# Kernel optimization log

Hardware: AMD Instinct MI355X
Metric: run time of the kernel (lower is better)

Reference implementation:

```python
import jax, jax.numpy as jnp
import numpy as np

N_USERS = 100000
N_MOVIES = 20000
N_EDGES = 600000
FEAT = 64
HID = 128
OUT = 64
N_TUPLES = 100000


def _sage(x_src, x_dst, src_idx, dst_idx, n_dst, Wl, bl, Wr):
    # PyG SAGEConv (mean aggr): lin_l(mean of gathered src feats) + lin_r(x_dst)
    msg = x_src[src_idx]                                        # [E, d_src]
    summ = jax.ops.segment_sum(msg, dst_idx, num_segments=n_dst)
    cnt = jax.ops.segment_sum(jnp.ones((src_idx.shape[0],), x_src.dtype),
                              dst_idx, num_segments=n_dst)
    mean = summ / jnp.maximum(cnt, 1.0)[:, None]
    return mean @ Wl.T + bl + x_dst @ Wr.T


def setup_inputs() -> dict:
    key = jax.random.key(0)
    ks = jax.random.split(key, 20)
    s = 0.05
    return {
        "movie_x": jax.random.normal(ks[0], (N_MOVIES, FEAT), jnp.float32),
        "user_idx": jax.random.randint(ks[1], (N_EDGES,), 0, N_USERS),
        "movie_idx": jax.random.randint(ks[2], (N_EDGES,), 0, N_MOVIES),
        "tuples_coo": jax.random.randint(ks[3], (2, N_TUPLES), 0, N_MOVIES),
        "user_emb": jax.random.normal(ks[4], (1, HID), jnp.float32) * s,
        "W1l": jax.random.normal(ks[5], (HID, FEAT), jnp.float32) * s,
        "b1": jnp.zeros((HID,), jnp.float32),
        "W1r": jax.random.normal(ks[6], (HID, HID), jnp.float32) * s,
        "W2l": jax.random.normal(ks[7], (HID, HID), jnp.float32) * s,
        "b2": jnp.zeros((HID,), jnp.float32),
        "W2r": jax.random.normal(ks[8], (HID, FEAT), jnp.float32) * s,
        "W3l": jax.random.normal(ks[9], (HID, HID), jnp.float32) * s,
        "b3": jnp.zeros((HID,), jnp.float32),
        "W3r": jax.random.normal(ks[10], (HID, HID), jnp.float32) * s,
        "Wlin1": jax.random.normal(ks[11], (OUT, HID), jnp.float32) * s,
        "blin1": jnp.zeros((OUT,), jnp.float32),
        "Wlin2": jax.random.normal(ks[12], (OUT, HID), jnp.float32) * s,
        "blin2": jnp.zeros((OUT,), jnp.float32),
    }


def reference(movie_x, user_idx, movie_idx, tuples_coo, user_emb,
              W1l, b1, W1r, W2l, b2, W2r, W3l, b3, W3r,
              Wlin1, blin1, Wlin2, blin2):
    n_users = N_USERS
    user_x0 = jnp.broadcast_to(user_emb, (n_users, HID))  # emb.weight.repeat
    # conv1: (movie -> user) rev_rates edges: src=movie_idx, dst=user_idx
    user_x = jax.nn.relu(_sage(movie_x, user_x0, movie_idx, user_idx, n_users, W1l, b1, W1r))
    # conv2: (user -> movie) rates edges: src=user_idx, dst=movie_idx
    movie_z = jax.nn.relu(_sage(user_x, movie_x, user_idx, movie_idx, N_MOVIES, W2l, b2, W2r))
    # conv3: (movie -> user) again
    user_z = jax.nn.relu(_sage(movie_z, user_x, movie_idx, user_idx, n_users, W3l, b3, W3r))
    z_user = user_z @ Wlin1.T + blin1
    z_movie = movie_z @ Wlin2.T + blin2
    X = jnp.vstack((z_user, z_movie))
    # relation_schema = ['user', 'movie']: offset movie indices by n_users
    new_index = jnp.vstack((tuples_coo[0], tuples_coo[1] + n_users))
    return X, new_index
```

## Files before the change

kernel.cpp:

```cpp
#include <hip/hip_runtime.h>

typedef __attribute__((ext_vector_type(8))) short short8;
typedef __attribute__((ext_vector_type(4))) float f32x4;

static const int NU = 100000;
static const int NM = 20000;
static const int NE = 600000;
static const int FEAT = 64;
static const int HID = 128;
static const int OUTD = 64;
static const int NTOT = NU + NM;
static const int NLIST = 2 * NE;
static const int CVT_TOT = 81920 + NM * FEAT;
static const int CVT_BLKS = (CVT_TOT + 255) / 256;
static const int IDX_BLKS = (100000 + 255) / 256;

static const int UB_SHIFT = 9;
static const int MB_SHIFT = 7;
static const int NBU = (NU + 511) >> 9;
static const int NBM = (NM + 127) >> 7;
static const int NBUCK = NBU + NBM;
static const int EPB = 4096;
static const int NPBLK = (NE + EPB - 1) / EPB;

__device__ inline float b2f(unsigned short h) {
    unsigned int u = ((unsigned int)h) << 16;
    float f; __builtin_memcpy(&f, &u, 4); return f;
}
__device__ inline unsigned short f2b(float f) {
    unsigned int u; __builtin_memcpy(&u, &f, 4);
    u += 0x7FFFu + ((u >> 16) & 1u);
    return (unsigned short)(u >> 16);
}
__device__ inline unsigned int pk2(float a, float b) {
    return (unsigned int)f2b(a) | ((unsigned int)f2b(b) << 16);
}
__device__ inline int wswz(int row, int bc, int rowbytes) {
    return row * rowbytes + (bc ^ ((row & 7) << 4));
}

__global__ __launch_bounds__(256) void k_hist(const int* __restrict__ ui,
                                              const int* __restrict__ mi,
                                              int* __restrict__ ghist) {
    __shared__ int h[NBUCK];
    const int tid = threadIdx.x;
    for (int i = tid; i < NBUCK; i += 256) h[i] = 0;
    __syncthreads();
#pragma unroll
    for (int it = 0; it < EPB / 256; ++it) {
        int e = blockIdx.x * EPB + it * 256 + tid;
        if (e < NE) {
            atomicAdd(&h[ui[e] >> UB_SHIFT], 1);
            atomicAdd(&h[NBU + (mi[e] >> MB_SHIFT)], 1);
        }
    }
    __syncthreads();
    for (int i = tid; i < NBUCK; i += 256)
        if (h[i]) atomicAdd(&ghist[i], h[i]);
}

__global__ __launch_bounds__(512) void k_bscan(const int* __restrict__ ghist,
                                               int* __restrict__ bb,
                                               int* __restrict__ gcur) {
    __shared__ int s[512];
    const int tid = threadIdx.x;
    int v = (tid < NBUCK) ? ghist[tid] : 0;
    s[tid] = v;
    __syncthreads();
#pragma unroll
    for (int off = 1; off < 512; off <<= 1) {
        int x = (tid >= off) ? s[tid - off] : 0;
        __syncthreads();
        s[tid] += x;
        __syncthreads();
    }
    int excl = s[tid] - v;
    if (tid < NBUCK) { bb[tid] = excl; gcur[tid] = excl; }
    if (tid == 511) bb[NBUCK] = s[511];
}

__global__ __launch_bounds__(256) void k_part(const int* __restrict__ ui,
                                              const int* __restrict__ mi,
                                              int* __restrict__ gcur,
                                              int* __restrict__ entries) {
    __shared__ int h[NBUCK], base[NBUCK], cur[NBUCK];
    const int tid = threadIdx.x;
    for (int i = tid; i < NBUCK; i += 256) h[i] = 0;
    __syncthreads();

    int eu[EPB / 256], em[EPB / 256];
#pragma unroll
    for (int it = 0; it < EPB / 256; ++it) {
        int e = blockIdx.x * EPB + it * 256 + tid;
        if (e < NE) {
            eu[it] = ui[e]; em[it] = mi[e];
            atomicAdd(&h[eu[it] >> UB_SHIFT], 1);
            atomicAdd(&h[NBU + (em[it] >> MB_SHIFT)], 1);
        } else eu[it] = -1;
    }
    __syncthreads();
    for (int i = tid; i < NBUCK; i += 256) {
        int c = h[i];
        base[i] = c ? atomicAdd(&gcur[i], c) : 0;
        cur[i] = 0;
    }
    __syncthreads();
#pragma unroll
    for (int it = 0; it < EPB / 256; ++it) {
        if (eu[it] < 0) continue;
        int u = eu[it], m = em[it];
        int bu = u >> UB_SHIFT;
        int o1 = base[bu] + atomicAdd(&cur[bu], 1);
        entries[o1] = (m << UB_SHIFT) | (u & 511);
        int bm = NBU + (m >> MB_SHIFT);
        int o2 = base[bm] + atomicAdd(&cur[bm], 1);
        entries[o2] = (u << MB_SHIFT) | (m & 127);
    }
}

__global__ __launch_bounds__(256) void k_csr(const int* __restrict__ bb,
                                             const int* __restrict__ entries,
                                             int* __restrict__ rp,
                                             int* __restrict__ list) {
    __shared__ int lcnt[512], lrp[512], lcur[512], ps[256];
    const int b = blockIdx.x;
    const int tid = threadIdx.x;
    const int s = bb[b], e = bb[b + 1];
    const bool isU = b < NBU;
    const int shift = isU ? UB_SHIFT : MB_SHIFT;
    const int mask = isU ? 511 : 127;
    const int n0 = isU ? (b << UB_SHIFT) : ((b - NBU) << MB_SHIFT);
    const int nNodes = isU ? min(512, NU - n0) : min(128, NM - n0);
    const int g0 = isU ? n0 : NU + n0;

    for (int i = tid; i < 512; i += 256) { lcnt[i] = 0; lcur[i] = 0; }
    __syncthreads();
    for (int i = s + tid; i < e; i += 256)
        atomicAdd(&lcnt[entries[i] & mask], 1);
    __syncthreads();
    int a0 = lcnt[2 * tid], a1 = lcnt[2 * tid + 1];
    int pr = a0 + a1;
    ps[tid] = pr;
    __syncthreads();
#pragma unroll
    for (int off = 1; off < 256; off <<= 1) {
        int x = (tid >= off) ? ps[tid - off] : 0;
        __syncthreads();
        ps[tid] += x;
        __syncthreads();
    }
    int excl = ps[tid] - pr;
    lrp[2 * tid] = excl;
    lrp[2 * tid + 1] = excl + a0;
    __syncthreads();
    for (int i = tid; i < nNodes; i += 256) rp[g0 + i] = s + lrp[i];
    if (b == NBUCK - 1 && tid == 0) rp[NTOT] = e;
    for (int i = s + tid; i < e; i += 256) {
        int p = entries[i];
        int dl = p & mask;
        int off = s + lrp[dl] + atomicAdd(&lcur[dl], 1);
        list[off] = p >> shift;
    }
}

__global__ void k_misc(const float* __restrict__ w1l, const float* __restrict__ w2l,
                       const float* __restrict__ w2r, const float* __restrict__ w3l,
                       const float* __restrict__ w3r, const float* __restrict__ wl1,
                       const float* __restrict__ wl2, const float* __restrict__ mx,
                       unsigned short* __restrict__ dst,
                       const int* __restrict__ tpl, float* __restrict__ oidx,
                       const float* __restrict__ ue, const float* __restrict__ w1r,
                       const float* __restrict__ b1, float* __restrict__ c1) {
    const int b = blockIdx.x;
    if (b < CVT_BLKS) {
        int g = b * 256 + threadIdx.x;
        if (g >= CVT_TOT) return;
        const float* s; int o;
        if      (g < 8192)   { s = w1l; o = g; }
        else if (g < 24576)  { s = w2l; o = g - 8192; }
        else if (g < 32768)  { s = w2r; o = g - 24576; }
        else if (g < 49152)  { s = w3l; o = g - 32768; }
        else if (g < 65536)  { s = w3r; o = g - 49152; }
        else if (g < 73728)  { s = wl1; o = g - 65536; }
        else if (g < 81920)  { s = wl2; o = g - 73728; }
        else                 { s = mx;  o = g - 81920; }
        dst[g] = f2b(s[o]);
    } else if (b < CVT_BLKS + IDX_BLKS) {
        int i = (b - CVT_BLKS) * 256 + threadIdx.x;
        if (i < 100000) {
            oidx[i] = (float)tpl[i];
            oidx[100000 + i] = (float)(tpl[100000 + i] + NU);
        }
    } else {
        int h = threadIdx.x;
        if (h < HID) {
            float a = 0.f;
#pragma unroll 16
            for (int k = 0; k < HID; ++k) a += ue[k] * w1r[h * HID + k];
            c1[h] = a + b1[h];
        }
    }
}

template<int C>
__global__ __launch_bounds__(256) void k_gather_b(const unsigned short* __restrict__ src,
                                                  const int* __restrict__ rp,
                                                  const int* __restrict__ list,
                                                  unsigned short* __restrict__ dst,
                                                  int base, int n) {
    constexpr int TPN = C / 8;
    constexpr int NPB = 256 / TPN;
    const int node = blockIdx.x * NPB + threadIdx.x / TPN;
    if (node >= n) return;
    const int c8 = (threadIdx.x % TPN) * 8;
    const int g = base + node;
    const int s = rp[g], e = rp[g + 1];

    float a[8];
#pragma unroll
    for (int j = 0; j < 8; ++j) a[j] = 0.f;

    int i = s;
    for (; i + 1 < e; i += 2) {
        int r0 = list[i], r1 = list[i + 1];
        short8 v0 = *reinterpret_cast<const short8*>(src + (size_t)r0 * C + c8);
        short8 v1 = *reinterpret_cast<const short8*>(src + (size_t)r1 * C + c8);
#pragma unroll
        for (int j = 0; j < 8; ++j)
            a[j] += b2f((unsigned short)v0[j]) + b2f((unsigned short)v1[j]);
    }
    if (i < e) {
        int r0 = list[i];
        short8 v0 = *reinterpret_cast<const short8*>(src + (size_t)r0 * C + c8);
#pragma unroll
        for (int j = 0; j < 8; ++j) a[j] += b2f((unsigned short)v0[j]);
    }
    const float sc = 1.0f / (float)max(e - s, 1);
    short8 o;
#pragma unroll
    for (int j = 0; j < 8; ++j) o[j] = (short)f2b(a[j] * sc);
    *reinterpret_cast<short8*>(dst + (size_t)node * C + c8) = o;
}

template<int K, int NO, bool AVEC, bool RELU, bool F32OUT>
__global__ __launch_bounds__(256) void k_mf2(const unsigned short* __restrict__ X,
                                             const unsigned short* __restrict__ W,
                                             const float* __restrict__ vec,
                                             void* __restrict__ Yv, int M) {
    constexpr int KT = K / 32;
    constexpr int CG = NO / 16;
    constexpr int WB = NO * K * 2;
    constexpr int RB = K * 2;
    __shared__ __align__(16) char lds[WB];
    const int tid = threadIdx.x;
    const int lane = tid & 63;
    const int wv = tid >> 6;
    const int rbase = blockIdx.x * 128 + wv * 32;
    const int lr = lane & 15;
    const int kg = lane >> 4;

#pragma unroll
    for (int i = 0; i < WB / 16 / 256; ++i) {
        int idx = tid + i * 256;
        int row = idx / (RB / 16);
        int bc = (idx % (RB / 16)) * 16;
        *reinterpret_cast<uint4*>(lds + wswz(row, bc, RB)) =
            *reinterpret_cast<const uint4*>((const char*)W + idx * 16);
    }

    short8 xb[2][KT];
#pragma unroll
    for (int t = 0; t < 2; ++t) {
        int row = min(rbase + t * 16 + lr, M - 1);
#pragma unroll
        for (int kt = 0; kt < KT; ++kt)
            xb[t][kt] = *reinterpret_cast<const short8*>(
                X + (size_t)row * K + kt * 32 + kg * 8);
    }
    __syncthreads();

    f32x4 acc[2][CG];
#pragma unroll
    for (int t = 0; t < 2; ++t)
#pragma unroll
        for (int c = 0; c < CG; ++c) acc[t][c] = (f32x4){0.f, 0.f, 0.f, 0.f};

#pragma unroll
    for (int cg = 0; cg < CG; ++cg) {
        short8 wf[KT];
#pragma unroll
        for (int kt = 0; kt < KT; ++kt)
            wf[kt] = *reinterpret_cast<const short8*>(
                lds + wswz(cg * 16 + lr, kt * 64 + kg * 16, RB));
#pragma unroll
        for (int kt = 0; kt < KT; ++kt)
#pragma unroll
            for (int t = 0; t < 2; ++t)
                acc[t][cg] = __builtin_amdgcn_mfma_f32_16x16x32_bf16(
                    wf[kt], xb[t][kt], acc[t][cg], 0, 0, 0);
    }

#pragma unroll
    for (int t = 0; t < 2; ++t) {
        const int u = rbase + t * 16 + lr;
        if (u >= M) continue;
#pragma unroll
        for (int cg = 0; cg < CG; ++cg) {
            const int h0 = cg * 16 + kg * 4;
            float v[4];
#pragma unroll
            for (int r = 0; r < 4; ++r) v[r] = acc[t][cg][r];
            if (AVEC) {
                float4 vv = *reinterpret_cast<const float4*>(vec + h0);
                v[0] += vv.x; v[1] += vv.y; v[2] += vv.z; v[3] += vv.w;
            }
            if (RELU)
#pragma unroll
                for (int r = 0; r < 4; ++r) v[r] = fmaxf(v[r], 0.f);
            if (F32OUT) {
                float4 o = make_float4(v[0], v[1], v[2], v[3]);
                *reinterpret_cast<float4*>((float*)Yv + (size_t)u * NO + h0) = o;
            } else {
                uint2 o = make_uint2(pk2(v[0], v[1]), pk2(v[2], v[3]));
                *reinterpret_cast<uint2*>((unsigned short*)Yv + (size_t)u * NO + h0) = o;
            }
        }
    }
}

__global__ __launch_bounds__(256) void k_fused_u(
        const unsigned short* __restrict__ mean3, const unsigned short* __restrict__ user_x,
        const unsigned short* __restrict__ W3l, const unsigned short* __restrict__ W3r,
        const float* __restrict__ b3, const unsigned short* __restrict__ Wl1,
        const float* __restrict__ bl1, float* __restrict__ out, int M) {
    __shared__ __align__(16) char lds[65536];
    const int tid = threadIdx.x;
    const int lane = tid & 63;
    const int wv = tid >> 6;
    const int rbase = blockIdx.x * 128 + wv * 32;
    const int lr = lane & 15;
    const int kg = lane >> 4;

#pragma unroll
    for (int i = 0; i < 8; ++i) {
        int idx = tid + i * 256;
        int row = idx >> 4, bc = (idx & 15) << 4;
        int sw = wswz(row, bc, 256);
        *reinterpret_cast<uint4*>(lds + sw) =
            *reinterpret_cast<const uint4*>((const char*)W3l + idx * 16);
        *reinterpret_cast<uint4*>(lds + 32768 + sw) =
            *reinterpret_cast<const uint4*>((const char*)W3r + idx * 16);
    }

    short8 xa[2][4], xc[2][4];
#pragma unroll
    for (int t = 0; t < 2; ++t) {
        int row = min(rbase + t * 16 + lr, M - 1);
#pragma unroll
        for (int kt = 0; kt < 4; ++kt) {
            xa[t][kt] = *reinterpret_cast<const short8*>(
                mean3 + (size_t)row * HID + kt * 32 + kg * 8);
            xc[t][kt] = *reinterpret_cast<const short8*>(
                user_x + (size_t)row * HID + kt * 32 + kg * 8);
        }
    }
    __syncthreads();

    f32x4 acc[2][8];
#pragma unroll
    for (int t = 0; t < 2; ++t)
#pragma unroll
        for (int c = 0; c < 8; ++c) acc[t][c] = (f32x4){0.f, 0.f, 0.f, 0.f};

#pragma unroll
    for (int cg = 0; cg < 8; ++cg) {
        short8 wl[4], wr[4];
#pragma unroll
        for (int kt = 0; kt < 4; ++kt) {
            int sw = wswz(cg * 16 + lr, kt * 64 + kg * 16, 256);
            wl[kt] = *reinterpret_cast<const short8*>(lds + sw);
            wr[kt] = *reinterpret_cast<const short8*>(lds + 32768 + sw);
        }
#pragma unroll
        for (int kt = 0; kt < 4; ++kt)
#pragma unroll
            for (int t = 0; t < 2; ++t) {
                acc[t][cg] = __builtin_amdgcn_mfma_f32_16x16x32_bf16(
                    wl[kt], xa[t][kt], acc[t][cg], 0, 0, 0);
                acc[t][cg] = __builtin_amdgcn_mfma_f32_16x16x32_bf16(
                    wr[kt], xc[t][kt], acc[t][cg], 0, 0, 0);
            }
    }
    __syncthreads();

#pragma unroll
    for (int i = 0; i < 4; ++i) {
        int idx = tid + i * 256;
        int row = idx >> 4, bc = (idx & 15) << 4;
        *reinterpret_cast<uint4*>(lds + 32768 + wswz(row, bc, 256)) =
            *reinterpret_cast<const uint4*>((const char*)Wl1 + idx * 16);
    }
#pragma unroll
    for (int t = 0; t < 2; ++t) {
        const int ul = wv * 32 + t * 16 + lr;
#pragma unroll
        for (int cg = 0; cg < 8; ++cg) {
            const int h0 = cg * 16 + kg * 4;
            float4 vv = *reinterpret_cast<const float4*>(b3 + h0);
            float v0 = fmaxf(acc[t][cg][0] + vv.x, 0.f);
            float v1 = fmaxf(acc[t][cg][1] + vv.y, 0.f);
            float v2 = fmaxf(acc[t][cg][2] + vv.z, 0.f);
            float v3 = fmaxf(acc[t][cg][3] + vv.w, 0.f);
            uint2 pk = make_uint2(pk2(v0, v1), pk2(v2, v3));
            *reinterpret_cast<uint2*>(lds + wswz(ul, h0 * 2, 256)) = pk;
        }
    }
    __syncthreads();

    short8 zb[2][4];
#pragma unroll
    for (int t = 0; t < 2; ++t) {
        const int ul = wv * 32 + t * 16 + lr;
#pragma unroll
        for (int kt = 0; kt < 4; ++kt)
            zb[t][kt] = *reinterpret_cast<const short8*>(
                lds + wswz(ul, kt * 64 + kg * 16, 256));
    }
    f32x4 a2[2][4];
#pragma unroll
    for (int t = 0; t < 2; ++t)
#pragma unroll
        for (int c = 0; c < 4; ++c) a2[t][c] = (f32x4){0.f, 0.f, 0.f, 0.f};
#pragma unroll
    for (int cg = 0; cg < 4; ++cg) {
        short8 wf[4];
#pragma unroll
        for (int kt = 0; kt < 4; ++kt)
            wf[kt] = *reinterpret_cast<const short8*>(
                lds + 32768 + wswz(cg * 16 + lr, kt * 64 + kg * 16, 256));
#pragma unroll
        for (int kt = 0; kt < 4; ++kt)
#pragma unroll
            for (int t = 0; t < 2; ++t)
                a2[t][cg] = __builtin_amdgcn_mfma_f32_16x16x32_bf16(
                    wf[kt], zb[t][kt], a2[t][cg], 0, 0, 0);
    }
#pragma unroll
    for (int t = 0; t < 2; ++t) {
        const int u = rbase + t * 16 + lr;
        if (u >= M) continue;
#pragma unroll
        for (int cg = 0; cg < 4; ++cg) {
            const int o0 = cg * 16 + kg * 4;
            float4 bb = *reinterpret_cast<const float4*>(bl1 + o0);
            float4 o = make_float4(a2[t][cg][0] + bb.x, a2[t][cg][1] + bb.y,
                                   a2[t][cg][2] + bb.z, a2[t][cg][3] + bb.w);
            *reinterpret_cast<float4*>(out + (size_t)u * OUTD + o0) = o;
        }
    }
}

__global__ __launch_bounds__(256) void k_fused_m(
        const unsigned short* __restrict__ mean2, const unsigned short* __restrict__ mxb,
        const unsigned short* __restrict__ W2l, const unsigned short* __restrict__ W2r,
        const float* __restrict__ b2, unsigned short* __restrict__ movie_z,
        const unsigned short* __restrict__ Wl2, const float* __restrict__ bl2,
        float* __restrict__ out, int M) {
    __shared__ __align__(16) char lds[49152];
    const int tid = threadIdx.x;
    const int lane = tid & 63;
    const int wv = tid >> 6;
    const int rbase = blockIdx.x * 128 + wv * 32;
    const int lr = lane & 15;
    const int kg = lane >> 4;

#pragma unroll
    for (int i = 0; i < 8; ++i) {
        int idx = tid + i * 256;
        int row = idx >> 4, bc = (idx & 15) << 4;
        *reinterpret_cast<uint4*>(lds + wswz(row, bc, 256)) =
            *reinterpret_cast<const uint4*>((const char*)W2l + idx * 16);
    }
#pragma unroll
    for (int i = 0; i < 4; ++i) {
        int idx = tid + i * 256;
        int row = idx >> 3, bc = (idx & 7) << 4;
        *reinterpret_cast<uint4*>(lds + 32768 + wswz(row, bc, 128)) =
            *reinterpret_cast<const uint4*>((const char*)W2r + idx * 16);
    }

    short8 xa[2][4], xc[2][2];
#pragma unroll
    for (int t = 0; t < 2; ++t) {
        int row = min(rbase + t * 16 + lr, M - 1);
#pragma unroll
        for (int kt = 0; kt < 4; ++kt)
            xa[t][kt] = *reinterpret_cast<const short8*>(
                mean2 + (size_t)row * HID + kt * 32 + kg * 8);
#pragma unroll
        for (int kt = 0; kt < 2; ++kt)
            xc[t][kt] = *reinterpret_cast<const short8*>(
                mxb + (size_t)row * FEAT + kt * 32 + kg * 8);
    }
    __syncthreads();

    f32x4 acc[2][8];
#pragma unroll
    for (int t = 0; t < 2; ++t)
#pragma unroll
        for (int c = 0; c < 8; ++c) acc[t][c] = (f32x4){0.f, 0.f, 0.f, 0.f};

#pragma unroll
    for (int cg = 0; cg < 8; ++cg) {
        short8 wl[4], wr[2];
#pragma unroll
        for (int kt = 0; kt < 4; ++kt)
            wl[kt] = *reinterpret_cast<const short8*>(
                lds + wswz(cg * 16 + lr, kt * 64 + kg * 16, 256));
#pragma unroll
        for (int kt = 0; kt < 2; ++kt)
            wr[kt] = *reinterpret_cast<const short8*>(
                lds + 32768 + wswz(cg * 16 + lr, kt * 64 + kg * 16, 128));
#pragma unroll
        for (int kt = 0; kt < 4; ++kt)
#pragma unroll
            for (int t = 0; t < 2; ++t)
                acc[t][cg] = __builtin_amdgcn_mfma_f32_16x16x32_bf16(
                    wl[kt], xa[t][kt], acc[t][cg], 0, 0, 0);
#pragma unroll
        for (int kt = 0; kt < 2; ++kt)
#pragma unroll
            for (int t = 0; t < 2; ++t)
                acc[t][cg] = __builtin_amdgcn_mfma_f32_16x16x32_bf16(
                    wr[kt], xc[t][kt], acc[t][cg], 0, 0, 0);
    }
    __syncthreads();

#pragma unroll
    for (int i = 0; i < 4; ++i) {
        int idx = tid + i * 256;
        int row = idx >> 4, bc = (idx & 15) << 4;
        *reinterpret_cast<uint4*>(lds + 32768 + wswz(row, bc, 256)) =
            *reinterpret_cast<const uint4*>((const char*)Wl2 + idx * 16);
    }
#pragma unroll
    for (int t = 0; t < 2; ++t) {
        const int ul = wv * 32 + t * 16 + lr;
        const int u = rbase + t * 16 + lr;
#pragma unroll
        for (int cg = 0; cg < 8; ++cg) {
            const int h0 = cg * 16 + kg * 4;
            float4 vv = *reinterpret_cast<const float4*>(b2 + h0);
            float v0 = fmaxf(acc[t][cg][0] + vv.x, 0.f);
            float v1 = fmaxf(acc[t][cg][1] + vv.y, 0.f);
            float v2 = fmaxf(acc[t][cg][2] + vv.z, 0.f);
            float v3 = fmaxf(acc[t][cg][3] + vv.w, 0.f);
            uint2 pk = make_uint2(pk2(v0, v1), pk2(v2, v3));
            *reinterpret_cast<uint2*>(lds + wswz(ul, h0 * 2, 256)) = pk;
            if (u < M)
                *reinterpret_cast<uint2*>(movie_z + (size_t)u * HID + h0) = pk;
        }
    }
    __syncthreads();

    short8 zb[2][4];
#pragma unroll
    for (int t = 0; t < 2; ++t) {
        const int ul = wv * 32 + t * 16 + lr;
#pragma unroll
        for (int kt = 0; kt < 4; ++kt)
            zb[t][kt] = *reinterpret_cast<const short8*>(
                lds + wswz(ul, kt * 64 + kg * 16, 256));
    }
    f32x4 a2[2][4];
#pragma unroll
    for (int t = 0; t < 2; ++t)
#pragma unroll
        for (int c = 0; c < 4; ++c) a2[t][c] = (f32x4){0.f, 0.f, 0.f, 0.f};
#pragma unroll
    for (int cg = 0; cg < 4; ++cg) {
        short8 wf[4];
#pragma unroll
        for (int kt = 0; kt < 4; ++kt)
            wf[kt] = *reinterpret_cast<const short8*>(
                lds + 32768 + wswz(cg * 16 + lr, kt * 64 + kg * 16, 256));
#pragma unroll
        for (int kt = 0; kt < 4; ++kt)
#pragma unroll
            for (int t = 0; t < 2; ++t)
                a2[t][cg] = __builtin_amdgcn_mfma_f32_16x16x32_bf16(
                    wf[kt], zb[t][kt], a2[t][cg], 0, 0, 0);
    }
#pragma unroll
    for (int t = 0; t < 2; ++t) {
        const int u = rbase + t * 16 + lr;
        if (u >= M) continue;
#pragma unroll
        for (int cg = 0; cg < 4; ++cg) {
            const int o0 = cg * 16 + kg * 4;
            float4 bb = *reinterpret_cast<const float4*>(bl2 + o0);
            float4 o = make_float4(a2[t][cg][0] + bb.x, a2[t][cg][1] + bb.y,
                                   a2[t][cg][2] + bb.z, a2[t][cg][3] + bb.w);
            *reinterpret_cast<float4*>(out + (size_t)u * OUTD + o0) = o;
        }
    }
}

extern "C" void kernel_launch(void* const* d_in, const int* in_sizes, int n_in,
                              void* d_out, int out_size, void* d_ws, size_t ws_size,
                              hipStream_t stream) {
    const float* movie_x  = (const float*)d_in[0];
    const int*   user_idx = (const int*)d_in[1];
    const int*   movie_idx= (const int*)d_in[2];
    const int*   tuples   = (const int*)d_in[3];
    const float* user_emb = (const float*)d_in[4];
    const float* W1l = (const float*)d_in[5];
    const float* b1  = (const float*)d_in[6];
    const float* W1r = (const float*)d_in[7];
    const float* W2l = (const float*)d_in[8];
    const float* b2  = (const float*)d_in[9];
    const float* W2r = (const float*)d_in[10];
    const float* W3l = (const float*)d_in[11];
    const float* b3  = (const float*)d_in[12];
    const float* W3r = (const float*)d_in[13];
    const float* Wlin1 = (const float*)d_in[14];
    const float* blin1 = (const float*)d_in[15];
    const float* Wlin2 = (const float*)d_in[16];
    const float* blin2 = (const float*)d_in[17];

    float* out = (float*)d_out;

    char* p = (char*)d_ws;
    int* ghist = (int*)p;  p += 360 * 4;
    int* bb    = (int*)p;  p += 360 * 4;
    int* gcur  = (int*)p;  p += 360 * 4;
    int* entries = (int*)p; p += (size_t)NLIST * 4;
    int* rp    = (int*)p;  p += (size_t)(NTOT + 8) * 4;
    int* list  = (int*)p;  p += (size_t)NLIST * 4;
    float* c1  = (float*)p; p += 128 * 4;
    unsigned short* wb = (unsigned short*)p; p += (size_t)CVT_TOT * 2;
    unsigned short* W1l_b  = wb;
    unsigned short* W2l_b  = wb + 8192;
    unsigned short* W2r_b  = wb + 24576;
    unsigned short* W3l_b  = wb + 32768;
    unsigned short* W3r_b  = wb + 49152;
    unsigned short* Wlin1_b= wb + 65536;
    unsigned short* Wlin2_b= wb + 73728;
    unsigned short* mxb    = wb + 81920;
    unsigned short* mean1  = (unsigned short*)p; p += (size_t)NU * FEAT * 2;
    unsigned short* user_x = (unsigned short*)p; p += (size_t)NU * HID * 2;
    unsigned short* mean2  = (unsigned short*)p; p += (size_t)NM * HID * 2;
    unsigned short* movie_z= (unsigned short*)p; p += (size_t)NM * HID * 2;
    unsigned short* mean3  = (unsigned short*)p; p += (size_t)NU * HID * 2;

    hipMemsetAsync(ghist, 0, NBUCK * sizeof(int), stream);
    k_hist<<<NPBLK, 256, 0, stream>>>(user_idx, movie_idx, ghist);
    k_bscan<<<1, 512, 0, stream>>>(ghist, bb, gcur);
    k_part<<<NPBLK, 256, 0, stream>>>(user_idx, movie_idx, gcur, entries);
    k_csr<<<NBUCK, 256, 0, stream>>>(bb, entries, rp, list);

    k_misc<<<CVT_BLKS + IDX_BLKS + 1, 256, 0, stream>>>(
        W1l, W2l, W2r, W3l, W3r, Wlin1, Wlin2, movie_x, wb,
        tuples, out + (size_t)(NU + NM) * OUTD, user_emb, W1r, b1, c1);

    k_gather_b<FEAT><<<(NU + 31) / 32, 256, 0, stream>>>(mxb, rp, list, mean1, 0, NU);
    k_mf2<FEAT, HID, true, true, false><<<(NU + 127) / 128, 256, 0, stream>>>(
        mean1, W1l_b, c1, user_x, NU);

    k_gather_b<HID><<<(NM + 15) / 16, 256, 0, stream>>>(user_x, rp, list, mean2, NU, NM);
    k_fused_m<<<(NM + 127) / 128, 256, 0, stream>>>(
        mean2, mxb, W2l_b, W2r_b, b2, movie_z, Wlin2_b, blin2,
        out + (size_t)NU * OUTD, NM);

    k_gather_b<HID><<<(NU + 15) / 16, 256, 0, stream>>>(movie_z, rp, list, mean3, 0, NU);
    k_fused_u<<<(NU + 127) / 128, 256, 0, stream>>>(
        mean3, user_x, W3l_b, W3r_b, b3, Wlin1_b, blin1, out, NU);
}
```

Before: 183.2 us.

## Apply W3l before aggregation on movies and merge hist with misc kernel

Layer-3 lin_l is moved ahead of the mean aggregation. The movie kernel now computes Y3 = movie_z·W3l^T for the 20k movies, and the user kernel adds the gathered mean of Y3 directly, dropping the 128x128 W3l GEMM over 100k users. The histogram kernel and the weight-conversion/index kernel are merged into one launch to save a launch. Costs are an extra GEMM and store in the movie kernel plus an added bf16 rounding of Y3 before averaging.

```diff
diff --git a/kernel.cpp b/kernel.cpp
--- a/kernel.cpp
+++ b/kernel.cpp
@@ -39,24 +39,61 @@
     return row * rowbytes + (bc ^ ((row & 7) << 4));
 }
 
-__global__ __launch_bounds__(256) void k_hist(const int* __restrict__ ui,
-                                              const int* __restrict__ mi,
-                                              int* __restrict__ ghist) {
+__global__ __launch_bounds__(256) void k_hist_misc(
+        const int* __restrict__ ui, const int* __restrict__ mi, int* __restrict__ ghist,
+        const float* __restrict__ w1l, const float* __restrict__ w2l,
+        const float* __restrict__ w2r, const float* __restrict__ w3l,
+        const float* __restrict__ w3r, const float* __restrict__ wl1,
+        const float* __restrict__ wl2, const float* __restrict__ mx,
+        unsigned short* __restrict__ dst,
+        const int* __restrict__ tpl, float* __restrict__ oidx,
+        const float* __restrict__ ue, const float* __restrict__ w1r,
+        const float* __restrict__ b1, float* __restrict__ c1) {
     __shared__ int h[NBUCK];
+    const int b = blockIdx.x;
     const int tid = threadIdx.x;
-    for (int i = tid; i < NBUCK; i += 256) h[i] = 0;
-    __syncthreads();
-#pragma unroll
-    for (int it = 0; it < EPB / 256; ++it) {
-        int e = blockIdx.x * EPB + it * 256 + tid;
-        if (e < NE) {
-            atomicAdd(&h[ui[e] >> UB_SHIFT], 1);
-            atomicAdd(&h[NBU + (mi[e] >> MB_SHIFT)], 1);
-        }
-    }
-    __syncthreads();
-    for (int i = tid; i < NBUCK; i += 256)
-        if (h[i]) atomicAdd(&ghist[i], h[i]);
+    if (b < NPBLK) {
+        for (int i = tid; i < NBUCK; i += 256) h[i] = 0;
+        __syncthreads();
+#pragma unroll
+        for (int it = 0; it < EPB / 256; ++it) {
+            int e = b * EPB + it * 256 + tid;
+            if (e < NE) {
+                atomicAdd(&h[ui[e] >> UB_SHIFT], 1);
+                atomicAdd(&h[NBU + (mi[e] >> MB_SHIFT)], 1);
+            }
+        }
+        __syncthreads();
+        for (int i = tid; i < NBUCK; i += 256)
+            if (h[i]) atomicAdd(&ghist[i], h[i]);
+    } else if (b < NPBLK + CVT_BLKS) {
+        int g = (b - NPBLK) * 256 + tid;
+        if (g >= CVT_TOT) return;
+        const float* s; int o;
+        if      (g < 8192)   { s = w1l; o = g; }
+        else if (g < 24576)  { s = w2l; o = g - 8192; }
+        else if (g < 32768)  { s = w2r; o = g - 24576; }
+        else if (g < 49152)  { s = w3l; o = g - 32768; }
+        else if (g < 65536)  { s = w3r; o = g - 49152; }
+        else if (g < 73728)  { s = wl1; o = g - 65536; }
+        else if (g < 81920)  { s = wl2; o = g - 73728; }
+        else                 { s = mx;  o = g - 81920; }
+        dst[g] = f2b(s[o]);
+    } else if (b < NPBLK + CVT_BLKS + IDX_BLKS) {
+        int i = (b - NPBLK - CVT_BLKS) * 256 + tid;
+        if (i < 100000) {
+            oidx[i] = (float)tpl[i];
+            oidx[100000 + i] = (float)(tpl[100000 + i] + NU);
+        }
+    } else {
+        int hh = tid;
+        if (hh < HID) {
+            float a = 0.f;
+#pragma unroll 16
+            for (int k = 0; k < HID; ++k) a += ue[k] * w1r[hh * HID + k];
+            c1[hh] = a + b1[hh];
+        }
+    }
 }
 
 __global__ __launch_bounds__(512) void k_bscan(const int* __restrict__ ghist,
@@ -160,45 +197,6 @@
         int dl = p & mask;
         int off = s + lrp[dl] + atomicAdd(&lcur[dl], 1);
         list[off] = p >> shift;
-    }
-}
-
-__global__ void k_misc(const float* __restrict__ w1l, const float* __restrict__ w2l,
-                       const float* __restrict__ w2r, const float* __restrict__ w3l,
-                       const float* __restrict__ w3r, const float* __restrict__ wl1,
-                       const float* __restrict__ wl2, const float* __restrict__ mx,
-                       unsigned short* __restrict__ dst,
-                       const int* __restrict__ tpl, float* __restrict__ oidx,
-                       const float* __restrict__ ue, const float* __restrict__ w1r,
-                       const float* __restrict__ b1, float* __restrict__ c1) {
-    const int b = blockIdx.x;
-    if (b < CVT_BLKS) {
-        int g = b * 256 + threadIdx.x;
-        if (g >= CVT_TOT) return;
-        const float* s; int o;
-        if      (g < 8192)   { s = w1l; o = g; }
-        else if (g < 24576)  { s = w2l; o = g - 8192; }
-        else if (g < 32768)  { s = w2r; o = g - 24576; }
-        else if (g < 49152)  { s = w3l; o = g - 32768; }
-        else if (g < 65536)  { s = w3r; o = g - 49152; }
-        else if (g < 73728)  { s = wl1; o = g - 65536; }
-        else if (g < 81920)  { s = wl2; o = g - 73728; }
-        else                 { s = mx;  o = g - 81920; }
-        dst[g] = f2b(s[o]);
-    } else if (b < CVT_BLKS + IDX_BLKS) {
-        int i = (b - CVT_BLKS) * 256 + threadIdx.x;
-        if (i < 100000) {
-            oidx[i] = (float)tpl[i];
-            oidx[100000 + i] = (float)(tpl[100000 + i] + NU);
-        }
-    } else {
-        int h = threadIdx.x;
-        if (h < HID) {
-            float a = 0.f;
-#pragma unroll 16
-            for (int k = 0; k < HID; ++k) a += ue[k] * w1r[h * HID + k];
-            c1[h] = a + b1[h];
-        }
     }
 }
 
@@ -329,142 +327,9 @@
 }
 
 __global__ __launch_bounds__(256) void k_fused_u(
-        const unsigned short* __restrict__ mean3, const unsigned short* __restrict__ user_x,
-        const unsigned short* __restrict__ W3l, const unsigned short* __restrict__ W3r,
-        const float* __restrict__ b3, const unsigned short* __restrict__ Wl1,
-        const float* __restrict__ bl1, float* __restrict__ out, int M) {
-    __shared__ __align__(16) char lds[65536];
-    const int tid = threadIdx.x;
-    const int lane = tid & 63;
-    const int wv = tid >> 6;
-    const int rbase = blockIdx.x * 128 + wv * 32;
-    const int lr = lane & 15;
-    const int kg = lane >> 4;
-
-#pragma unroll
-    for (int i = 0; i < 8; ++i) {
-        int idx = tid + i * 256;
-        int row = idx >> 4, bc = (idx & 15) << 4;
-        int sw = wswz(row, bc, 256);
-        *reinterpret_cast<uint4*>(lds + sw) =
-            *reinterpret_cast<const uint4*>((const char*)W3l + idx * 16);
-        *reinterpret_cast<uint4*>(lds + 32768 + sw) =
-            *reinterpret_cast<const uint4*>((const char*)W3r + idx * 16);
-    }
-
-    short8 xa[2][4], xc[2][4];
-#pragma unroll
-    for (int t = 0; t < 2; ++t) {
-        int row = min(rbase + t * 16 + lr, M - 1);
-#pragma unroll
-        for (int kt = 0; kt < 4; ++kt) {
-            xa[t][kt] = *reinterpret_cast<const short8*>(
-                mean3 + (size_t)row * HID + kt * 32 + kg * 8);
-            xc[t][kt] = *reinterpret_cast<const short8*>(
-                user_x + (size_t)row * HID + kt * 32 + kg * 8);
-        }
-    }
-    __syncthreads();
-
-    f32x4 acc[2][8];
-#pragma unroll
-    for (int t = 0; t < 2; ++t)
-#pragma unroll
-        for (int c = 0; c < 8; ++c) acc[t][c] = (f32x4){0.f, 0.f, 0.f, 0.f};
-
-#pragma unroll
-    for (int cg = 0; cg < 8; ++cg) {
-        short8 wl[4], wr[4];
-#pragma unroll
-        for (int kt = 0; kt < 4; ++kt) {
-            int sw = wswz(cg * 16 + lr, kt * 64 + kg * 16, 256);
-            wl[kt] = *reinterpret_cast<const short8*>(lds + sw);
-            wr[kt] = *reinterpret_cast<const short8*>(lds + 32768 + sw);
-        }
-#pragma unroll
-        for (int kt = 0; kt < 4; ++kt)
-#pragma unroll
-            for (int t = 0; t < 2; ++t) {
-                acc[t][cg] = __builtin_amdgcn_mfma_f32_16x16x32_bf16(
-                    wl[kt], xa[t][kt], acc[t][cg], 0, 0, 0);
-                acc[t][cg] = __builtin_amdgcn_mfma_f32_16x16x32_bf16(
-                    wr[kt], xc[t][kt], acc[t][cg], 0, 0, 0);
-            }
-    }
-    __syncthreads();
-
-#pragma unroll
-    for (int i = 0; i < 4; ++i) {
-        int idx = tid + i * 256;
-        int row = idx >> 4, bc = (idx & 15) << 4;
-        *reinterpret_cast<uint4*>(lds + 32768 + wswz(row, bc, 256)) =
-            *reinterpret_cast<const uint4*>((const char*)Wl1 + idx * 16);
-    }
-#pragma unroll
-    for (int t = 0; t < 2; ++t) {
-        const int ul = wv * 32 + t * 16 + lr;
-#pragma unroll
-        for (int cg = 0; cg < 8; ++cg) {
-            const int h0 = cg * 16 + kg * 4;
-            float4 vv = *reinterpret_cast<const float4*>(b3 + h0);
-            float v0 = fmaxf(acc[t][cg][0] + vv.x, 0.f);
-            float v1 = fmaxf(acc[t][cg][1] + vv.y, 0.f);
-            float v2 = fmaxf(acc[t][cg][2] + vv.z, 0.f);
-            float v3 = fmaxf(acc[t][cg][3] + vv.w, 0.f);
-            uint2 pk = make_uint2(pk2(v0, v1), pk2(v2, v3));
-            *reinterpret_cast<uint2*>(lds + wswz(ul, h0 * 2, 256)) = pk;
-        }
-    }
-    __syncthreads();
-
-    short8 zb[2][4];
-#pragma unroll
-    for (int t = 0; t < 2; ++t) {
-        const int ul = wv * 32 + t * 16 + lr;
-#pragma unroll
-        for (int kt = 0; kt < 4; ++kt)
-            zb[t][kt] = *reinterpret_cast<const short8*>(
-                lds + wswz(ul, kt * 64 + kg * 16, 256));
-    }
-    f32x4 a2[2][4];
-#pragma unroll
-    for (int t = 0; t < 2; ++t)
-#pragma unroll
-        for (int c = 0; c < 4; ++c) a2[t][c] = (f32x4){0.f, 0.f, 0.f, 0.f};
-#pragma unroll
-    for (int cg = 0; cg < 4; ++cg) {
-        short8 wf[4];
-#pragma unroll
-        for (int kt = 0; kt < 4; ++kt)
-            wf[kt] = *reinterpret_cast<const short8*>(
-                lds + 32768 + wswz(cg * 16 + lr, kt * 64 + kg * 16, 256));
-#pragma unroll
-        for (int kt = 0; kt < 4; ++kt)
-#pragma unroll
-            for (int t = 0; t < 2; ++t)
-                a2[t][cg] = __builtin_amdgcn_mfma_f32_16x16x32_bf16(
-                    wf[kt], zb[t][kt], a2[t][cg], 0, 0, 0);
-    }
-#pragma unroll
-    for (int t = 0; t < 2; ++t) {
-        const int u = rbase + t * 16 + lr;
-        if (u >= M) continue;
-#pragma unroll
-        for (int cg = 0; cg < 4; ++cg) {
-            const int o0 = cg * 16 + kg * 4;
-            float4 bb = *reinterpret_cast<const float4*>(bl1 + o0);
-            float4 o = make_float4(a2[t][cg][0] + bb.x, a2[t][cg][1] + bb.y,
-                                   a2[t][cg][2] + bb.z, a2[t][cg][3] + bb.w);
-            *reinterpret_cast<float4*>(out + (size_t)u * OUTD + o0) = o;
-        }
-    }
-}
-
-__global__ __launch_bounds__(256) void k_fused_m(
-        const unsigned short* __restrict__ mean2, const unsigned short* __restrict__ mxb,
-        const unsigned short* __restrict__ W2l, const unsigned short* __restrict__ W2r,
-        const float* __restrict__ b2, unsigned short* __restrict__ movie_z,
-        const unsigned short* __restrict__ Wl2, const float* __restrict__ bl2,
+        const unsigned short* __restrict__ S3, const unsigned short* __restrict__ user_x,
+        const unsigned short* __restrict__ W3r, const float* __restrict__ b3,
+        const unsigned short* __restrict__ Wl1, const float* __restrict__ bl1,
         float* __restrict__ out, int M) {
     __shared__ __align__(16) char lds[49152];
     const int tid = threadIdx.x;
@@ -479,6 +344,131 @@
         int idx = tid + i * 256;
         int row = idx >> 4, bc = (idx & 15) << 4;
         *reinterpret_cast<uint4*>(lds + wswz(row, bc, 256)) =
+            *reinterpret_cast<const uint4*>((const char*)W3r + idx * 16);
+    }
+#pragma unroll
+    for (int i = 0; i < 4; ++i) {
+        int idx = tid + i * 256;
+        int row = idx >> 4, bc = (idx & 15) << 4;
+        *reinterpret_cast<uint4*>(lds + 32768 + wswz(row, bc, 256)) =
+            *reinterpret_cast<const uint4*>((const char*)Wl1 + idx * 16);
+    }
+
+    short8 xc[2][4];
+#pragma unroll
+    for (int t = 0; t < 2; ++t) {
+        int row = min(rbase + t * 16 + lr, M - 1);
+#pragma unroll
+        for (int kt = 0; kt < 4; ++kt)
+            xc[t][kt] = *reinterpret_cast<const short8*>(
+                user_x + (size_t)row * HID + kt * 32 + kg * 8);
+    }
+    __syncthreads();
+
+    f32x4 acc[2][8];
+#pragma unroll
+    for (int t = 0; t < 2; ++t)
+#pragma unroll
+        for (int c = 0; c < 8; ++c) acc[t][c] = (f32x4){0.f, 0.f, 0.f, 0.f};
+
+#pragma unroll
+    for (int cg = 0; cg < 8; ++cg) {
+        short8 wr[4];
+#pragma unroll
+        for (int kt = 0; kt < 4; ++kt)
+            wr[kt] = *reinterpret_cast<const short8*>(
+                lds + wswz(cg * 16 + lr, kt * 64 + kg * 16, 256));
+#pragma unroll
+        for (int kt = 0; kt < 4; ++kt)
+#pragma unroll
+            for (int t = 0; t < 2; ++t)
+                acc[t][cg] = __builtin_amdgcn_mfma_f32_16x16x32_bf16(
+                    wr[kt], xc[t][kt], acc[t][cg], 0, 0, 0);
+    }
+    __syncthreads();
+
+#pragma unroll
+    for (int t = 0; t < 2; ++t) {
+        const int ul = wv * 32 + t * 16 + lr;
+        const int u = min(rbase + t * 16 + lr, M - 1);
+#pragma unroll
+        for (int cg = 0; cg < 8; ++cg) {
+            const int h0 = cg * 16 + kg * 4;
+            uint2 s3 = *reinterpret_cast<const uint2*>(S3 + (size_t)u * HID + h0);
+            float4 vv = *reinterpret_cast<const float4*>(b3 + h0);
+            float v0 = fmaxf(acc[t][cg][0] + b2f((unsigned short)(s3.x & 0xffff)) + vv.x, 0.f);
+            float v1 = fmaxf(acc[t][cg][1] + b2f((unsigned short)(s3.x >> 16)) + vv.y, 0.f);
+            float v2 = fmaxf(acc[t][cg][2] + b2f((unsigned short)(s3.y & 0xffff)) + vv.z, 0.f);
+            float v3 = fmaxf(acc[t][cg][3] + b2f((unsigned short)(s3.y >> 16)) + vv.w, 0.f);
+            uint2 pk = make_uint2(pk2(v0, v1), pk2(v2, v3));
+            *reinterpret_cast<uint2*>(lds + wswz(ul, h0 * 2, 256)) = pk;
+        }
+    }
+    __syncthreads();
+
+    short8 zb[2][4];
+#pragma unroll
+    for (int t = 0; t < 2; ++t) {
+        const int ul = wv * 32 + t * 16 + lr;
+#pragma unroll
+        for (int kt = 0; kt < 4; ++kt)
+            zb[t][kt] = *reinterpret_cast<const short8*>(
+                lds + wswz(ul, kt * 64 + kg * 16, 256));
+    }
+    f32x4 a2[2][4];
+#pragma unroll
+    for (int t = 0; t < 2; ++t)
+#pragma unroll
+        for (int c = 0; c < 4; ++c) a2[t][c] = (f32x4){0.f, 0.f, 0.f, 0.f};
+#pragma unroll
+    for (int cg = 0; cg < 4; ++cg) {
+        short8 wf[4];
+#pragma unroll
+        for (int kt = 0; kt < 4; ++kt)
+            wf[kt] = *reinterpret_cast<const short8*>(
+                lds + 32768 + wswz(cg * 16 + lr, kt * 64 + kg * 16, 256));
+#pragma unroll
+        for (int kt = 0; kt < 4; ++kt)
+#pragma unroll
+            for (int t = 0; t < 2; ++t)
+                a2[t][cg] = __builtin_amdgcn_mfma_f32_16x16x32_bf16(
+                    wf[kt], zb[t][kt], a2[t][cg], 0, 0, 0);
+    }
+#pragma unroll
+    for (int t = 0; t < 2; ++t) {
+        const int u = rbase + t * 16 + lr;
+        if (u >= M) continue;
+#pragma unroll
+        for (int cg = 0; cg < 4; ++cg) {
+            const int o0 = cg * 16 + kg * 4;
+            float4 bb = *reinterpret_cast<const float4*>(bl1 + o0);
+            float4 o = make_float4(a2[t][cg][0] + bb.x, a2[t][cg][1] + bb.y,
+                                   a2[t][cg][2] + bb.z, a2[t][cg][3] + bb.w);
+            *reinterpret_cast<float4*>(out + (size_t)u * OUTD + o0) = o;
+        }
+    }
+}
+
+__global__ __launch_bounds__(256) void k_fused_m(
+        const unsigned short* __restrict__ mean2, const unsigned short* __restrict__ mxb,
+        const unsigned short* __restrict__ W2l, const unsigned short* __restrict__ W2r,
+        const float* __restrict__ b2, unsigned short* __restrict__ movie_z,
+        const unsigned short* __restrict__ Wl2, const float* __restrict__ bl2,
+        const unsigned short* __restrict__ W3l, unsigned short* __restrict__ Y3,
+        float* __restrict__ out, int M) {
+    __shared__ __align__(16) char lds[65536];
+    const int tid = threadIdx.x;
+    const int lane = tid & 63;
+    const int wv = tid >> 6;
+    const int rbase = blockIdx.x * 128 + wv * 32;
+    const int lr = lane & 15;
+    const int kg = lane >> 4;
+
+#pragma unroll
+    for (int i = 0; i < 8; ++i) {
+        int idx = tid + i * 256;
+        int row = idx >> 4, bc = (idx & 15) << 4;
+        *reinterpret_cast<uint4*>(lds + wswz(row, bc, 256)) =
             *reinterpret_cast<const uint4*>((const char*)W2l + idx * 16);
     }
 #pragma unroll
@@ -487,6 +477,9 @@
         int row = idx >> 3, bc = (idx & 7) << 4;
         *reinterpret_cast<uint4*>(lds + 32768 + wswz(row, bc, 128)) =
             *reinterpret_cast<const uint4*>((const char*)W2r + idx * 16);
+        int row2 = idx >> 4, bc2 = (idx & 15) << 4;
+        *reinterpret_cast<uint4*>(lds + 49152 + wswz(row2, bc2, 256)) =
+            *reinterpret_cast<const uint4*>((const char*)Wl2 + idx * 16);
     }
 
     short8 xa[2][4], xc[2][2];
@@ -536,13 +529,6 @@
     }
     __syncthreads();
 
-#pragma unroll
-    for (int i = 0; i < 4; ++i) {
-        int idx = tid + i * 256;
-        int row = idx >> 4, bc = (idx & 15) << 4;
-        *reinterpret_cast<uint4*>(lds + 32768 + wswz(row, bc, 256)) =
-            *reinterpret_cast<const uint4*>((const char*)Wl2 + idx * 16);
-    }
 #pragma unroll
     for (int t = 0; t < 2; ++t) {
         const int ul = wv * 32 + t * 16 + lr;
@@ -583,7 +569,7 @@
 #pragma unroll
         for (int kt = 0; kt < 4; ++kt)
             wf[kt] = *reinterpret_cast<const short8*>(
-                lds + 32768 + wswz(cg * 16 + lr, kt * 64 + kg * 16, 256));
+                lds + 49152 + wswz(cg * 16 + lr, kt * 64 + kg * 16, 256));
 #pragma unroll
         for (int kt = 0; kt < 4; ++kt)
 #pragma unroll
@@ -602,6 +588,48 @@
             float4 o = make_float4(a2[t][cg][0] + bb.x, a2[t][cg][1] + bb.y,
                                    a2[t][cg][2] + bb.z, a2[t][cg][3] + bb.w);
             *reinterpret_cast<float4*>(out + (size_t)u * OUTD + o0) = o;
+        }
+    }
+    __syncthreads();
+
+#pragma unroll
+    for (int i = 0; i < 8; ++i) {
+        int idx = tid + i * 256;
+        int row = idx >> 4, bc = (idx & 15) << 4;
+        *reinterpret_cast<uint4*>(lds + 32768 + wswz(row, bc, 256)) =
+            *reinterpret_cast<const uint4*>((const char*)W3l + idx * 16);
+    }
+    __syncthreads();
+
+    f32x4 a3[2][8];
+#pragma unroll
+    for (int t = 0; t < 2; ++t)
+#pragma unroll
+        for (int c = 0; c < 8; ++c) a3[t][c] = (f32x4){0.f, 0.f, 0.f, 0.f};
+#pragma unroll
+    for (int cg = 0; cg < 8; ++cg) {
+        short8 wf[4];
+#pragma unroll
+        for (int kt = 0; kt < 4; ++kt)
+            wf[kt] = *reinterpret_cast<const short8*>(
+                lds + 32768 + wswz(cg * 16 + lr, kt * 64 + kg * 16, 256));
+#pragma unroll
+        for (int kt = 0; kt < 4; ++kt)
+#pragma unroll
+            for (int t = 0; t < 2; ++t)
+                a3[t][cg] = __builtin_amdgcn_mfma_f32_16x16x32_bf16(
+                    wf[kt], zb[t][kt], a3[t][cg], 0, 0, 0);
+    }
+#pragma unroll
+    for (int t = 0; t < 2; ++t) {
+        const int u = rbase + t * 16 + lr;
+        if (u >= M) continue;
+#pragma unroll
+        for (int cg = 0; cg < 8; ++cg) {
+            const int h0 = cg * 16 + kg * 4;
+            uint2 pk = make_uint2(pk2(a3[t][cg][0], a3[t][cg][1]),
+                                  pk2(a3[t][cg][2], a3[t][cg][3]));
+            *reinterpret_cast<uint2*>(Y3 + (size_t)u * HID + h0) = pk;
         }
     }
 }
@@ -651,28 +679,28 @@
     unsigned short* user_x = (unsigned short*)p; p += (size_t)NU * HID * 2;
     unsigned short* mean2  = (unsigned short*)p; p += (size_t)NM * HID * 2;
     unsigned short* movie_z= (unsigned short*)p; p += (size_t)NM * HID * 2;
-    unsigned short* mean3  = (unsigned short*)p; p += (size_t)NU * HID * 2;
+    unsigned short* Y3     = (unsigned short*)p; p += (size_t)NM * HID * 2;
+    unsigned short* S3     = (unsigned short*)p; p += (size_t)NU * HID * 2;
 
     hipMemsetAsync(ghist, 0, NBUCK * sizeof(int), stream);
-    k_hist<<<NPBLK, 256, 0, stream>>>(user_idx, movie_idx, ghist);
+    k_hist_misc<<<NPBLK + CVT_BLKS + IDX_BLKS + 1, 256, 0, stream>>>(
+        user_idx, movie_idx, ghist,
+        W1l, W2l, W2r, W3l, W3r, Wlin1, Wlin2, movie_x, wb,
+        tuples, out + (size_t)(NU + NM) * OUTD, user_emb, W1r, b1, c1);
     k_bscan<<<1, 512, 0, stream>>>(ghist, bb, gcur);
     k_part<<<NPBLK, 256, 0, stream>>>(user_idx, movie_idx, gcur, entries);
     k_csr<<<NBUCK, 256, 0, stream>>>(bb, entries, rp, list);
 
-    k_misc<<<CVT_BLKS + IDX_BLKS + 1, 256, 0, stream>>>(
-        W1l, W2l, W2r, W3l, W3r, Wlin1, Wlin2, movie_x, wb,
-        tuples, out + (size_t)(NU + NM) * OUTD, user_emb, W1r, b1, c1);
-
     k_gather_b<FEAT><<<(NU + 31) / 32, 256, 0, stream>>>(mxb, rp, list, mean1, 0, NU);
     k_mf2<FEAT, HID, true, true, false><<<(NU + 127) / 128, 256, 0, stream>>>(
         mean1, W1l_b, c1, user_x, NU);
 
     k_gather_b<HID><<<(NM + 15) / 16, 256, 0, stream>>>(user_x, rp, list, mean2, NU, NM);
     k_fused_m<<<(NM + 127) / 128, 256, 0, stream>>>(
-        mean2, mxb, W2l_b, W2r_b, b2, movie_z, Wlin2_b, blin2,
+        mean2, mxb, W2l_b, W2r_b, b2, movie_z, Wlin2_b, blin2, W3l_b, Y3,
         out + (size_t)NU * OUTD, NM);
 
-    k_gather_b<HID><<<(NU + 15) / 16, 256, 0, stream>>>(movie_z, rp, list, mean3, 0, NU);
+    k_gather_b<HID><<<(NU + 15) / 16, 256, 0, stream>>>(Y3, rp, list, S3, 0, NU);
     k_fused_u<<<(NU + 127) / 128, 256, 0, stream>>>(
-        mean3, user_x, W3l_b, W3r_b, b3, Wlin1_b, blin1, out, NU);
-}
+        S3, user_x, W3r_b, b3, Wlin1_b, blin1, out, NU);
+}
```

Result: faster. 167.2 us (-8.7%).
